# Kernel optimization log

Hardware: AMD Instinct MI355X
Metric: run time of the kernel (lower is better)

## Reference

```python
import jax, jax.numpy as jnp
import numpy as np

B, T, D = 4, 2048, 1024
H, KVH = 16, 4          # query heads, kv heads
HD = D // H             # head_dim = 64
R = 32                  # partial rope dims
ROPE_BASE = 10000.0
EPS = 1e-6


def rmsnorm(x, scale):
    # per-head RMSNorm over last dim, computed in fp32 like the torch code
    xf = x.astype(jnp.float32)
    norm = jax.lax.rsqrt(jnp.mean(xf * xf, axis=-1, keepdims=True) + EPS)
    return (xf * norm).astype(x.dtype) * scale


def apply_rope(x, cos, sin):
    # x: (B,T,H,HD); rotate first R dims, pass the rest through
    x_r, x_p = x[..., :R], x[..., R:]
    half = R // 2
    x1, x2 = x_r[..., :half], x_r[..., half:]
    rotated = jnp.concatenate([x1 * cos - x2 * sin, x1 * sin + x2 * cos], axis=-1)
    return jnp.concatenate([rotated, x_p], axis=-1)


def setup_inputs() -> dict:
    key = jax.random.key(0)
    ks = jax.random.split(key, 8)
    x = jax.random.normal(ks[0], (B, T, D), dtype=jnp.float32)
    # RoPE tables exactly as RotaryEmbedding.get_cos_sin
    inv_freq = 1.0 / (ROPE_BASE ** (jnp.arange(0, R, 2, dtype=jnp.float32) / R))
    t = jnp.arange(T, dtype=jnp.float32)
    freqs = jnp.outer(t, inv_freq)                      # (T, R/2)
    cos = jnp.cos(freqs)[None, :, None, :]              # (1,T,1,R/2)
    sin = jnp.sin(freqs)[None, :, None, :]
    s = 1.0 / np.sqrt(D)
    Wq = jax.random.normal(ks[1], (D, D), dtype=jnp.float32) * s
    Wk = jax.random.normal(ks[2], (KVH * HD, D), dtype=jnp.float32) * s
    Wv = jax.random.normal(ks[3], (KVH * HD, D), dtype=jnp.float32) * s
    Wo = jax.random.normal(ks[4], (D, D), dtype=jnp.float32) * s
    q_scale = jnp.ones((HD,), dtype=jnp.float32)
    k_scale = jnp.ones((HD,), dtype=jnp.float32)
    return {"x": x, "cos": cos, "sin": sin, "Wq": Wq, "Wk": Wk, "Wv": Wv,
            "Wo": Wo, "q_scale": q_scale, "k_scale": k_scale}


def reference(x, cos, sin, Wq, Wk, Wv, Wo, q_scale, k_scale):
    b, t, d = x.shape
    q = jnp.einsum('btd,ed->bte', x, Wq).reshape(b, t, H, HD)
    k = jnp.einsum('btd,ed->bte', x, Wk).reshape(b, t, KVH, HD)
    v = jnp.einsum('btd,ed->bte', x, Wv).reshape(b, t, KVH, HD)
    q = apply_rope(rmsnorm(q, q_scale), cos, sin)
    k = apply_rope(rmsnorm(k, k_scale), cos, sin)
    groups = H // KVH
    k = jnp.repeat(k, groups, axis=2)   # (b,t,H,HD), matches repeat_interleave dim=2
    v = jnp.repeat(v, groups, axis=2)
    q = q.transpose(0, 2, 1, 3)         # (b,H,t,HD)
    k = k.transpose(0, 2, 1, 3)
    v = v.transpose(0, 2, 1, 3)
    scores = jnp.einsum('bhqd,bhkd->bhqk', q, k) / np.sqrt(HD)
    causal = jnp.tril(jnp.ones((t, t), dtype=bool))
    scores = jnp.where(causal, scores, -jnp.inf)
    attn = jax.nn.softmax(scores, axis=-1)
    y = jnp.einsum('bhqk,bhkd->bhqd', attn, v)
    y = y.transpose(0, 2, 1, 3).reshape(b, t, d)
    return jnp.einsum('btd,ed->bte', y, Wo)
```

## Files before the change

### kernel.cpp

```cpp
#include <hip/hip_runtime.h>
#include <hip/hip_bf16.h>
#include <stdint.h>

typedef __attribute__((ext_vector_type(8)))  __bf16 bf16x8;
typedef __attribute__((ext_vector_type(4)))  float  f32x4;
typedef __attribute__((ext_vector_type(16))) float  f32x16;
typedef __hip_bfloat16 bf16_t;

#define T_SEQ 2048
#define D_MODEL 1024
#define N_HEADS 16
#define N_KV 4
#define HD 64
#define LDQKV 1536
#define KDIM 1024

__device__ inline void cvt16(const float4* __restrict__ g, int4* __restrict__ s) {
  float4 v0 = g[0], v1 = g[1], v2 = g[2], v3 = g[3];
  union { int4 i[2]; __hip_bfloat162 h[8]; } u;
  u.h[0] = __float22bfloat162_rn(make_float2(v0.x, v0.y));
  u.h[1] = __float22bfloat162_rn(make_float2(v0.z, v0.w));
  u.h[2] = __float22bfloat162_rn(make_float2(v1.x, v1.y));
  u.h[3] = __float22bfloat162_rn(make_float2(v1.z, v1.w));
  u.h[4] = __float22bfloat162_rn(make_float2(v2.x, v2.y));
  u.h[5] = __float22bfloat162_rn(make_float2(v2.z, v2.w));
  u.h[6] = __float22bfloat162_rn(make_float2(v3.x, v3.y));
  u.h[7] = __float22bfloat162_rn(make_float2(v3.z, v3.w));
  s[0] = u.i[0]; s[1] = u.i[1];
}

__device__ inline void storeC(bf16_t* p, float v) { *p = __float2bfloat16(v); }
__device__ inline void storeC(float* p, float v) { *p = v; }

__device__ inline void plswap(unsigned& a, unsigned& b) {
  asm volatile("v_permlane32_swap_b32 %0, %1" : "+v"(a), "+v"(b));
}

__device__ inline float fexp2(float x) {
  float r; asm("v_exp_f32 %0, %1" : "=v"(r) : "v"(x)); return r;
}
__device__ inline unsigned cvtpk(float lo, float hi) {
  unsigned r; asm("v_cvt_pk_bf16_f32 %0, %1, %2" : "=v"(r) : "v"(lo), "v"(hi));
  return r;
}

__device__ inline void gll16(const bf16_t* g, bf16_t* l) {
  __builtin_amdgcn_global_load_lds(
      (const __attribute__((address_space(1))) void*)g,
      (__attribute__((address_space(3))) void*)l, 16, 0, 0);
}

__global__ __launch_bounds__(256) void all_cvt(
    const float* __restrict__ x,
    const float* __restrict__ Wq, const float* __restrict__ Wk,
    const float* __restrict__ Wv, const float* __restrict__ Wo,
    bf16_t* __restrict__ xb, bf16_t* __restrict__ wqkvb,
    bf16_t* __restrict__ wob) {
  const int i = blockIdx.x * 256 + threadIdx.x;
  const float* s; bf16_t* d; int off;
  if (i < 524288)      { s = x;  d = xb;                   off = i; }
  else if (i < 589824) { s = Wq; d = wqkvb;                off = i - 524288; }
  else if (i < 606208) { s = Wk; d = wqkvb + 1024 * 1024;  off = i - 589824; }
  else if (i < 622592) { s = Wv; d = wqkvb + 1280 * 1024;  off = i - 606208; }
  else                 { s = Wo; d = wob;                  off = i - 622592; }
  cvt16((const float4*)s + off * 4, (int4*)d + off * 2);
}

template <int MODE, int NX, typename CT>
__global__ __launch_bounds__(256) void gemm_bb(
    const bf16_t* __restrict__ A, const bf16_t* __restrict__ W,
    CT* __restrict__ C, const int ldC,
    const float* __restrict__ cosb, const float* __restrict__ sinb,
    const float* __restrict__ qs, const float* __restrict__ ks,
    bf16_t* __restrict__ v_t)
{
  __shared__ bf16_t Smem[8192];
  bf16_t* As = Smem;
  bf16_t* Bs = Smem + 4096;
  const int tid = threadIdx.x;
  const int lane = tid & 63;
  const int wv = tid >> 6;
  const int wr = wv >> 1, wc = wv & 1;
  const int id  = (int)blockIdx.x;
  const int xcd = id & 7;
  const int seq = id >> 3;
  const int mp  = (seq / NX) * 8 + xcd;
  const int nt  = seq - (seq / NX) * NX;
  const int m0 = mp * 128;
  const int n0 = nt * 128;

  const int srow = lane >> 2;
  const int scol = (lane & 3) * 8;
  const bf16_t* gA = A + (size_t)(m0 + 32 * wv + srow) * KDIM + scol;
  const bf16_t* gB = W + (size_t)(n0 + 32 * wv + srow) * KDIM + scol;
  bf16_t* lA = As + wv * 1024;
  bf16_t* lB = Bs + wv * 1024;

  f32x4 acc[4][4];
#pragma unroll
  for (int m = 0; m < 4; ++m)
#pragma unroll
    for (int n = 0; n < 4; ++n)
      acc[m][n] = {0.f, 0.f, 0.f, 0.f};

  const int fr = lane & 15;
  const int fq = lane >> 4;

  for (int k0 = 0; k0 < KDIM; k0 += 32) {
    gll16(gA + k0, lA);
    gll16(gA + 16 * KDIM + k0, lA + 512);
    gll16(gB + k0, lB);
    gll16(gB + 16 * KDIM + k0, lB + 512);
    __syncthreads();
    bf16x8 af[4], bfv[4];
#pragma unroll
    for (int m = 0; m < 4; ++m)
      af[m] = *(const bf16x8*)(&As[(wr * 64 + m * 16 + fr) * 32 + fq * 8]);
#pragma unroll
    for (int n = 0; n < 4; ++n)
      bfv[n] = *(const bf16x8*)(&Bs[(wc * 64 + n * 16 + fr) * 32 + fq * 8]);
#pragma unroll
    for (int m = 0; m < 4; ++m)
#pragma unroll
      for (int n = 0; n < 4; ++n)
        acc[m][n] = __builtin_amdgcn_mfma_f32_16x16x32_bf16(af[m], bfv[n],
                                                            acc[m][n], 0, 0, 0);
    __syncthreads();
  }

  if (MODE == 0 || n0 < 1280) {
    if (MODE == 1) {
      const float* stab = (n0 < 1024) ? qs : ks;
      float sc0 = stab[fr], sc1 = stab[16 + fr], sc2 = stab[32 + fr], sc3 = stab[48 + fr];
#pragma unroll
      for (int m = 0; m < 4; ++m)
#pragma unroll
        for (int r = 0; r < 4; ++r) {
          const int row = m0 + wr * 64 + m * 16 + fq * 4 + r;
          const int t = row & (T_SEQ - 1);
          float ss = acc[m][0][r] * acc[m][0][r] + acc[m][1][r] * acc[m][1][r]
                   + acc[m][2][r] * acc[m][2][r] + acc[m][3][r] * acc[m][3][r];
          ss += __shfl_xor(ss, 1);
          ss += __shfl_xor(ss, 2);
          ss += __shfl_xor(ss, 4);
          ss += __shfl_xor(ss, 8);
          const float nrm = rsqrtf(ss * (1.f / 64.f) + 1e-6f);
          const float v0 = acc[m][0][r] * nrm * sc0;
          const float v1 = acc[m][1][r] * nrm * sc1;
          const float v2 = acc[m][2][r] * nrm * sc2;
          const float v3 = acc[m][3][r] * nrm * sc3;
          const float c = cosb[t * 16 + fr];
          const float s = sinb[t * 16 + fr];
          union { unsigned u; bf16_t hh[2]; } pa, pb;
          pa.u = cvtpk(v0 * c - v1 * s, v0 * s + v1 * c);
          pb.u = cvtpk(v2, v3);
          bf16_t* p = (bf16_t*)C + (size_t)row * ldC + n0 + wc * 64 + fr;
          p[0]  = pa.hh[0];
          p[16] = pa.hh[1];
          p[32] = pb.hh[0];
          p[48] = pb.hh[1];
        }
    } else {
#pragma unroll
      for (int m = 0; m < 4; ++m)
#pragma unroll
        for (int n = 0; n < 4; ++n)
#pragma unroll
          for (int r = 0; r < 4; ++r) {
            const int row = wr * 64 + m * 16 + fq * 4 + r;
            const int col = wc * 64 + n * 16 + fr;
            storeC(&C[(size_t)(m0 + row) * ldC + n0 + col], acc[m][n][r]);
          }
    }
  } else {
    const int b4 = (m0 >> 11) * 4;
    const int t0base = m0 & (T_SEQ - 1);
    const int vcol = tid & 127;
    const int vc = n0 - 1280 + vcol;
    const int g = b4 + (vc >> 6);
    const int d = vc & 63;
#pragma unroll
    for (int half = 0; half < 2; ++half) {
      if (wr == half) {
#pragma unroll
        for (int m = 0; m < 4; ++m)
#pragma unroll
          for (int n = 0; n < 4; ++n)
#pragma unroll
            for (int r2 = 0; r2 < 4; r2 += 2) {
              union { unsigned u; bf16_t hh[2]; } pk2;
              pk2.u = cvtpk(acc[m][n][r2], acc[m][n][r2 + 1]);
              const int tl0 = m * 16 + fq * 4 + r2;
              const int col = wc * 64 + n * 16 + fr;
              const int sw = ((tl0 >> 2) & 7) << 4;
              Smem[tl0 * 128 + (col ^ sw)]       = pk2.hh[0];
              Smem[(tl0 + 1) * 128 + (col ^ sw)] = pk2.hh[1];
            }
      }
      __syncthreads();
      bf16_t* dst0 = v_t + ((size_t)(g * HD + d)) * T_SEQ + t0base + half * 64;
#pragma unroll
      for (int ci = 0; ci < 2; ++ci) {
        const int cu = (tid >> 7) + ci * 2;
        union { int4 q[2]; bf16_t hh[16]; } ld;
#pragma unroll
        for (int t = 0; t < 16; ++t) {
          const int tt = cu * 16 + t;
          ld.hh[t] = Smem[tt * 128 + (vcol ^ (((tt >> 2) & 7) << 4))];
        }
        *(int4*)(dst0 + cu * 16)     = ld.q[0];
        *(int4*)(dst0 + cu * 16 + 8) = ld.q[1];
      }
      __syncthreads();
    }
  }
}

__global__ __launch_bounds__(512) void attn(
    const bf16_t* __restrict__ qkv, const bf16_t* __restrict__ v_t,
    bf16_t* __restrict__ y)
{
  __shared__ int4 lds[2048];
  const int tid  = threadIdx.x;
  const int lane = tid & 63;
  const int w    = tid >> 6;
  const int spair= w >> 1;
  const int h    = w & 1;
  const int ql   = lane & 31;
  const int hi   = lane >> 5;
  const int id   = (int)blockIdx.x;
  const int low3 = id & 7;
  const int rest = id >> 3;
  const int gsel = rest & 1;
  const int hh   = (rest >> 1) & 3;
  const int sbi  = rest >> 3;
  const int sb   = ((sbi >> 2) & 1) ? (sbi + 4 - ((sbi >> 3) << 4)) : (15 - sbi);
  const int g16  = low3 + 8 * gsel;
  const int b    = g16 >> 2, kvh = g16 & 3;
  const int hd   = kvh * 4 + hh;
  const int s    = 4 * sb + spair;
  const int q_glob = s * 32 + ql;
  const int nt   = s + 1;
  const int nR   = 2 * sb + 2;
  const float SCALE_LOG2 = 0.125f * 1.44269504089f;

  const int sid = tid & 255;
  const int u   = tid >> 8;
  const int kr = sid >> 3, kslot = sid & 7;
  const int vd = sid >> 2, vslot = sid & 3;
  const bf16_t* gK = qkv + (size_t)(b * T_SEQ + kr + u * 32) * LDQKV + 1024 + kvh * HD + kslot * 8;
  const bf16_t* gV = v_t + (size_t)((b * N_KV + kvh) * HD + vd) * T_SEQ + vslot * 8 + u * 32;
  const int wKidx = u * 256 + kr * 8 + (kslot ^ (kr & 7));
  const int wVidx = 512 + u * 256 + vd * 4 + (vslot ^ ((vd >> 1) & 3));

  int kridx[4];
#pragma unroll
  for (int c = 0; c < 4; ++c)
    kridx[c] = ql * 8 + ((2 * c + hi) ^ (ql & 7));
  const int vsw = (ql >> 1) & 3;
  const int v0idx = 512 + ql * 4 + (hi ^ vsw);
  const int v1idx = 512 + ql * 4 + ((2 + hi) ^ vsw);
  const int v2idx = 512 + (ql + 32) * 4 + (hi ^ vsw);
  const int v3idx = 512 + (ql + 32) * 4 + ((2 + hi) ^ vsw);

  union ob { unsigned uu[4]; bf16x8 v; } onesf;
#pragma unroll
  for (int i = 0; i < 4; ++i) onesf.uu[i] = 0x3F803F80u;

  f32x16 zro;
#pragma unroll
  for (int i = 0; i < 16; ++i) zro[i] = 0.f;

  float* lf = (float*)lds;

  const bf16_t* Qrow = qkv + (size_t)(b * T_SEQ + q_glob) * LDQKV + hd * HD + hi * 8;
  bf16x8 qfrag[4];
#pragma unroll
  for (int c = 0; c < 4; ++c) {
    bf16x8 raw = *(const bf16x8*)(Qrow + c * 16);
    bf16x8 sc;
#pragma unroll
    for (int j = 0; j < 8; ++j)
      sc[j] = (__bf16)((float)raw[j] * SCALE_LOG2);
    qfrag[c] = sc;
  }

  f32x16 acc0, acc1, accL;
#pragma unroll
  for (int i = 0; i < 16; ++i) { acc0[i] = 0.f; acc1[i] = 0.f; accL[i] = 0.f; }
  float m_run = -1e30f;

  {
    int4 kA = *(const int4*)gK;
    int4 vA = *(const int4*)gV;
    lds[wKidx] = kA;
    lds[wVidx] = vA;
  }
  __syncthreads();

  int buf = 0;
  for (int r = 0; r < nR; ++r) {
    int4 kA, vA;
    const bool more = (r + 1 < nR);
    if (more) {
      kA = *(const int4*)(gK + (size_t)(r + 1) * 64 * LDQKV);
      vA = *(const int4*)(gV + (r + 1) * 64);
    }

    const int t = 2 * r + h;
    if (t < nt) {
      const int k0 = t << 5;
      const bool masked = (t == nt - 1);
      const int base = buf * 1024 + h * 256;

      bf16x8 kf0 = *(const bf16x8*)&lds[base + kridx[0]];
      bf16x8 kf1 = *(const bf16x8*)&lds[base + kridx[1]];
      bf16x8 kf2 = *(const bf16x8*)&lds[base + kridx[2]];
      bf16x8 kf3 = *(const bf16x8*)&lds[base + kridx[3]];

      __builtin_amdgcn_s_setprio(1);
      f32x16 st = __builtin_amdgcn_mfma_f32_32x32x16_bf16(kf0, qfrag[0], zro, 0, 0, 0);
      st = __builtin_amdgcn_mfma_f32_32x32x16_bf16(kf1, qfrag[1], st, 0, 0, 0);
      st = __builtin_amdgcn_mfma_f32_32x32x16_bf16(kf2, qfrag[2], st, 0, 0, 0);
      st = __builtin_amdgcn_mfma_f32_32x32x16_bf16(kf3, qfrag[3], st, 0, 0, 0);
      __builtin_amdgcn_s_setprio(0);

      if (masked) {
#pragma unroll
        for (int rr = 0; rr < 16; ++rr) {
          const int kg = k0 + (rr & 3) + 8 * (rr >> 2) + 4 * hi;
          if (kg > q_glob) st[rr] = -1e30f;
        }
      }
      float m01 = fmaxf(fmaxf(st[0], st[1]), st[2]);
      float m02 = fmaxf(fmaxf(st[3], st[4]), st[5]);
      float m03 = fmaxf(fmaxf(st[6], st[7]), st[8]);
      float m04 = fmaxf(fmaxf(st[9], st[10]), st[11]);
      float m05 = fmaxf(fmaxf(st[12], st[13]), st[14]);
      float m06 = fmaxf(fmaxf(m01, m02), m03);
      float m07 = fmaxf(fmaxf(m04, m05), st[15]);
      const float bmax = fmaxf(m06, m07);
      if (__any(bmax > m_run + 8.f)) {
        const float rmax = fmaxf(bmax, __shfl_xor(bmax, 32));
        const float mnew = fmaxf(m_run, rmax);
        const float corr = fexp2(m_run - mnew);
#pragma unroll
        for (int i = 0; i < 16; ++i) { acc0[i] *= corr; acc1[i] *= corr; }
        accL[0] *= corr;
        m_run = mnew;
      }
      float pp[16];
#pragma unroll
      for (int rr = 0; rr < 16; ++rr) pp[rr] = fexp2(st[rr] - m_run);

      unsigned wp[8];
#pragma unroll
      for (int i = 0; i < 8; ++i) wp[i] = cvtpk(pp[2 * i], pp[2 * i + 1]);
      plswap(wp[0], wp[2]); plswap(wp[1], wp[3]);
      plswap(wp[4], wp[6]); plswap(wp[5], wp[7]);
      union fu { unsigned uu2[4]; bf16x8 v; };
      fu f1, f2;
      f1.uu2[0] = wp[0]; f1.uu2[1] = wp[1]; f1.uu2[2] = wp[2]; f1.uu2[3] = wp[3];
      f2.uu2[0] = wp[4]; f2.uu2[1] = wp[5]; f2.uu2[2] = wp[6]; f2.uu2[3] = wp[7];

      bf16x8 vf0 = *(const bf16x8*)&lds[base + v0idx];
      bf16x8 vf1 = *(const bf16x8*)&lds[base + v1idx];
      bf16x8 vf2 = *(const bf16x8*)&lds[base + v2idx];
      bf16x8 vf3 = *(const bf16x8*)&lds[base + v3idx];

      __builtin_amdgcn_s_setprio(1);
      acc0 = __builtin_amdgcn_mfma_f32_32x32x16_bf16(vf0, f1.v, acc0, 0, 0, 0);
      acc0 = __builtin_amdgcn_mfma_f32_32x32x16_bf16(vf1, f2.v, acc0, 0, 0, 0);
      acc1 = __builtin_amdgcn_mfma_f32_32x32x16_bf16(vf2, f1.v, acc1, 0, 0, 0);
      acc1 = __builtin_amdgcn_mfma_f32_32x32x16_bf16(vf3, f2.v, acc1, 0, 0, 0);
      accL = __builtin_amdgcn_mfma_f32_32x32x16_bf16(onesf.v, f1.v, accL, 0, 0, 0);
      accL = __builtin_amdgcn_mfma_f32_32x32x16_bf16(onesf.v, f2.v, accL, 0, 0, 0);
      __builtin_amdgcn_s_setprio(0);
    }

    if (more) {
      const int nb = (buf ^ 1) * 1024;
      lds[nb + wKidx] = kA;
      lds[nb + wVidx] = vA;
    }
    __syncthreads();
    buf ^= 1;
  }

  float cA = 1.f, cB = 0.f, l_mrg = 0.f;
  if (h == 1) {
    const int fb = spair * 1216 + lane * 19;
#pragma unroll
    for (int i = 0; i < 16; ++i) lf[fb + i] = acc0[i];
    lf[fb + 16] = m_run;
    lf[fb + 17] = accL[0];
  }
  __syncthreads();
  if (h == 0) {
    const int fb = spair * 1216 + lane * 19;
    const float mB = lf[fb + 16], lB = lf[fb + 17];
    const float mM = fmaxf(m_run, mB);
    cA = fexp2(m_run - mM);
    cB = fexp2(mB - mM);
    l_mrg = accL[0] * cA + lB * cB;
#pragma unroll
    for (int i = 0; i < 16; ++i) acc0[i] = acc0[i] * cA + lf[fb + i] * cB;
  }
  __syncthreads();
  if (h == 1) {
    const int fb2 = spair * 1088 + lane * 17;
#pragma unroll
    for (int i = 0; i < 16; ++i) lf[fb2 + i] = acc1[i];
  }
  __syncthreads();
  if (h == 0) {
    const int fb2 = spair * 1088 + lane * 17;
#pragma unroll
    for (int i = 0; i < 16; ++i) acc1[i] = acc1[i] * cA + lf[fb2 + i] * cB;
    const float inv = 1.f / l_mrg;
    bf16_t* yrow = y + (size_t)(b * T_SEQ + q_glob) * D_MODEL + hd * HD;
#pragma unroll
    for (int gg = 0; gg < 4; ++gg) {
      uint2 o0, o1;
      o0.x = cvtpk(acc0[4 * gg + 0] * inv, acc0[4 * gg + 1] * inv);
      o0.y = cvtpk(acc0[4 * gg + 2] * inv, acc0[4 * gg + 3] * inv);
      o1.x = cvtpk(acc1[4 * gg + 0] * inv, acc1[4 * gg + 1] * inv);
      o1.y = cvtpk(acc1[4 * gg + 2] * inv, acc1[4 * gg + 3] * inv);
      *(uint2*)(yrow + 8 * gg + 4 * hi)      = o0;
      *(uint2*)(yrow + 32 + 8 * gg + 4 * hi) = o1;
    }
  }
}

extern "C" void kernel_launch(void* const* d_in, const int* in_sizes, int n_in,
                              void* d_out, int out_size, void* d_ws,
                              size_t ws_size, hipStream_t stream) {
  const float* x    = (const float*)d_in[0];
  const float* cosb = (const float*)d_in[1];
  const float* sinb = (const float*)d_in[2];
  const float* Wq   = (const float*)d_in[3];
  const float* Wk   = (const float*)d_in[4];
  const float* Wv   = (const float*)d_in[5];
  const float* Wo   = (const float*)d_in[6];
  const float* qs   = (const float*)d_in[7];
  const float* ks   = (const float*)d_in[8];
  float* out = (float*)d_out;

  char* ws = (char*)d_ws;
  bf16_t* qkv   = (bf16_t*)ws;
  bf16_t* v_t   = (bf16_t*)(ws + 25165824);
  bf16_t* y     = (bf16_t*)(ws + 29360128);
  bf16_t* xb    = y;
  bf16_t* wqkvb = (bf16_t*)(ws + 46137344);
  bf16_t* wob   = (bf16_t*)(ws + 49283072);

  all_cvt<<<dim3(2688), 256, 0, stream>>>(x, Wq, Wk, Wv, Wo, xb, wqkvb, wob);

  gemm_bb<1, 12, bf16_t><<<dim3(768), 256, 0, stream>>>(
      xb, wqkvb, qkv, LDQKV, cosb, sinb, qs, ks, v_t);
  attn<<<dim3(1024), 512, 0, stream>>>(qkv, v_t, y);
  gemm_bb<0, 8, float><<<dim3(512), 256, 0, stream>>>(
      y, wob, out, D_MODEL, nullptr, nullptr, nullptr, nullptr, nullptr);
}
```

Baseline: 149.3 us.

## Double-buffer GEMM LDS tiles and widen K step to 64

Replaces the single-buffered K loop in the bf16 GEMM with a two-stage LDS ping-pong. The next 64-wide K chunk is loaded by global_load_lds while MFMAs run on the current chunk, and the loop now needs one barrier per 64 K instead of two per 32. This hides global load latency and cuts synchronisation, but shared memory per block grows from 16 KB to 64 KB, which may lower occupancy.

```diff
diff --git a/kernel.cpp b/kernel.cpp
--- a/kernel.cpp
+++ b/kernel.cpp
@@ -74,9 +74,7 @@
     const float* __restrict__ qs, const float* __restrict__ ks,
     bf16_t* __restrict__ v_t)
 {
-  __shared__ bf16_t Smem[8192];
-  bf16_t* As = Smem;
-  bf16_t* Bs = Smem + 4096;
+  __shared__ bf16_t Smem[32768];
   const int tid = threadIdx.x;
   const int lane = tid & 63;
   const int wv = tid >> 6;
@@ -93,8 +91,7 @@
   const int scol = (lane & 3) * 8;
   const bf16_t* gA = A + (size_t)(m0 + 32 * wv + srow) * KDIM + scol;
   const bf16_t* gB = W + (size_t)(n0 + 32 * wv + srow) * KDIM + scol;
-  bf16_t* lA = As + wv * 1024;
-  bf16_t* lB = Bs + wv * 1024;
+  const int lOff = wv * 1024;
 
   f32x4 acc[4][4];
 #pragma unroll
@@ -106,27 +103,47 @@
   const int fr = lane & 15;
   const int fq = lane >> 4;
 
-  for (int k0 = 0; k0 < KDIM; k0 += 32) {
-    gll16(gA + k0, lA);
-    gll16(gA + 16 * KDIM + k0, lA + 512);
-    gll16(gB + k0, lB);
-    gll16(gB + 16 * KDIM + k0, lB + 512);
+#define STAGE_GEMM(bufb, kk) {                                        \
+    bf16_t* _bs = Smem + (bufb) * 16384 + lOff;                       \
+    gll16(gA + (kk), _bs);                                            \
+    gll16(gA + 16 * KDIM + (kk), _bs + 512);                          \
+    gll16(gA + (kk) + 32, _bs + 4096);                                \
+    gll16(gA + 16 * KDIM + (kk) + 32, _bs + 4608);                    \
+    gll16(gB + (kk), _bs + 8192);                                     \
+    gll16(gB + 16 * KDIM + (kk), _bs + 8704);                         \
+    gll16(gB + (kk) + 32, _bs + 12288);                               \
+    gll16(gB + 16 * KDIM + (kk) + 32, _bs + 12800);                   \
+  }
+
+  STAGE_GEMM(0, 0);
+  __syncthreads();
+
+  int buf = 0;
+  for (int r = 0; r < 16; ++r) {
+    if (r + 1 < 16) STAGE_GEMM(buf ^ 1, (r + 1) * 64);
+    const bf16_t* base = Smem + buf * 16384;
+#pragma unroll
+    for (int half = 0; half < 2; ++half) {
+      const bf16_t* As = base + half * 4096;
+      const bf16_t* Bs = base + 8192 + half * 4096;
+      bf16x8 af[4], bfv[4];
+#pragma unroll
+      for (int m = 0; m < 4; ++m)
+        af[m] = *(const bf16x8*)(&As[(wr * 64 + m * 16 + fr) * 32 + fq * 8]);
+#pragma unroll
+      for (int n = 0; n < 4; ++n)
+        bfv[n] = *(const bf16x8*)(&Bs[(wc * 64 + n * 16 + fr) * 32 + fq * 8]);
+#pragma unroll
+      for (int m = 0; m < 4; ++m)
+#pragma unroll
+        for (int n = 0; n < 4; ++n)
+          acc[m][n] = __builtin_amdgcn_mfma_f32_16x16x32_bf16(af[m], bfv[n],
+                                                              acc[m][n], 0, 0, 0);
+    }
     __syncthreads();
-    bf16x8 af[4], bfv[4];
-#pragma unroll
-    for (int m = 0; m < 4; ++m)
-      af[m] = *(const bf16x8*)(&As[(wr * 64 + m * 16 + fr) * 32 + fq * 8]);
-#pragma unroll
-    for (int n = 0; n < 4; ++n)
-      bfv[n] = *(const bf16x8*)(&Bs[(wc * 64 + n * 16 + fr) * 32 + fq * 8]);
-#pragma unroll
-    for (int m = 0; m < 4; ++m)
-#pragma unroll
-      for (int n = 0; n < 4; ++n)
-        acc[m][n] = __builtin_amdgcn_mfma_f32_16x16x32_bf16(af[m], bfv[n],
-                                                            acc[m][n], 0, 0, 0);
-    __syncthreads();
-  }
+    buf ^= 1;
+  }
+#undef STAGE_GEMM
 
   if (MODE == 0 || n0 < 1280) {
     if (MODE == 1) {
```

Measured after the change: 135.7 us, median of 2. -9.1%, faster.
